# Optimization experiments

Measured on AMD Instinct MI355X. Metric: run time of the kernel, lower is better.

## Reference

```python
import jax, jax.numpy as jnp
import numpy as np

B, T, D = 2, 2048, 2048
H, KV = 16, 4
HD = D // H  # 128
ROPE_BASE = 10000.0


def _rope(t):
    # t: [B, h, T, HD]; faithful to torch apply_rope (even/odd split, concat halves)
    pos = jnp.arange(T, dtype=t.dtype)
    inv_freq = 1.0 / (ROPE_BASE ** (jnp.arange(0, HD, 2, dtype=t.dtype) / HD))
    ang = jnp.einsum('t,f->tf', pos, inv_freq)  # [T, HD/2]
    sin = jnp.sin(ang)[None, None]
    cos = jnp.cos(ang)[None, None]
    t1, t2 = t[..., ::2], t[..., 1::2]
    return jnp.concatenate([t1 * cos - t2 * sin, t1 * sin + t2 * cos], axis=-1)


def setup_inputs() -> dict:
    key = jax.random.key(0)
    kx, kq, kk, kv, ko = jax.random.split(key, 5)
    x = jax.random.normal(kx, (B, T, D), dtype=jnp.float32)
    s = 0.02
    Wq = jax.random.normal(kq, (D, D), dtype=jnp.float32) * s
    Wk = jax.random.normal(kk, (D, KV * HD), dtype=jnp.float32) * s
    Wv = jax.random.normal(kv, (D, KV * HD), dtype=jnp.float32) * s
    Wo = jax.random.normal(ko, (D, D), dtype=jnp.float32) * s
    return {"x": x, "Wq": Wq, "Wk": Wk, "Wv": Wv, "Wo": Wo}


def reference(x, Wq, Wk, Wv, Wo):
    # projections (nn.Linear, no bias)
    q = (x @ Wq).reshape(B, T, H, HD).transpose(0, 2, 1, 3)    # [B,H,T,HD]
    k = (x @ Wk).reshape(B, T, KV, HD).transpose(0, 2, 1, 3)   # [B,KV,T,HD]
    v = (x @ Wv).reshape(B, T, KV, HD).transpose(0, 2, 1, 3)
    q = _rope(q)
    k = _rope(k)
    # GQA: repeat_interleave kv heads to full head count
    g = H // KV
    k = jnp.repeat(k, g, axis=1)
    v = jnp.repeat(v, g, axis=1)
    # causal SDPA, default scale 1/sqrt(head_dim)
    scale = 1.0 / jnp.sqrt(jnp.array(HD, dtype=x.dtype))
    scores = jnp.einsum('bhqd,bhkd->bhqk', q, k) * scale
    mask = jnp.tril(jnp.ones((T, T), dtype=bool))
    scores = jnp.where(mask, scores, jnp.finfo(scores.dtype).min)
    attn = jax.nn.softmax(scores, axis=-1)
    out = jnp.einsum('bhqk,bhkd->bhqd', attn, v)               # [B,H,T,HD]
    out = out.transpose(0, 2, 1, 3).reshape(B, T, D)
    return out @ Wo
```

## Files before the change

kernel.cpp:

```cpp
#include <hip/hip_runtime.h>
#include <math.h>

#define BB 2
#define TT 2048
#define DD 2048
#define HH 16
#define KVHN 4
#define HDIM 128
#define NKV 3072

typedef unsigned short u16;
typedef unsigned int u32;
typedef __bf16 bf16x8 __attribute__((ext_vector_type(8)));
typedef float  f32x4  __attribute__((ext_vector_type(4)));

#define AS1 __attribute__((address_space(1)))
#define AS3 __attribute__((address_space(3)))

__device__ __forceinline__ void dma16(const u16* g, u16* l) {
  __builtin_amdgcn_global_load_lds((const AS1 u32*)g, (AS3 u32*)l, 16, 0, 0);
}

__device__ __forceinline__ u16 f2bf(float f) {
  u32 u = __float_as_uint(f);
  u32 r = (u + 0x7FFFu + ((u >> 16) & 1u)) >> 16;
  return (u16)r;
}
__device__ __forceinline__ float bf2f(u32 h) { return __uint_as_float(h << 16); }

__device__ __forceinline__ u32 pack2(float a, float b) {
  union { __bf16 h[2]; u32 u; } cv;
  cv.h[0] = (__bf16)a; cv.h[1] = (__bf16)b;
  return cv.u;
}

__global__ __launch_bounds__(256) void castf2b(const float* __restrict__ in,
                                               u16* __restrict__ out) {
  size_t i4 = (size_t)blockIdx.x * 256 + threadIdx.x;
  float4 v = *(const float4*)(in + i4 * 4);
  ushort4 o;
  o.x = f2bf(v.x); o.y = f2bf(v.y); o.z = f2bf(v.z); o.w = f2bf(v.w);
  *(ushort4*)(out + i4 * 4) = o;
}

__global__ __launch_bounds__(256) void tcast(const float* __restrict__ W,
                                             u16* __restrict__ WT,
                                             int K, int N) {
  __shared__ float tile[32][33];
  const int n0 = blockIdx.x * 32, k0 = blockIdx.y * 32;
  const int r = threadIdx.x >> 3;
  const int c4 = (threadIdx.x & 7) * 4;
  float4 v = *(const float4*)(W + (size_t)(k0 + r) * N + n0 + c4);
  tile[r][c4 + 0] = v.x; tile[r][c4 + 1] = v.y;
  tile[r][c4 + 2] = v.z; tile[r][c4 + 3] = v.w;
  __syncthreads();
  ushort4 o;
  o.x = f2bf(tile[c4 + 0][r]); o.y = f2bf(tile[c4 + 1][r]);
  o.z = f2bf(tile[c4 + 2][r]); o.w = f2bf(tile[c4 + 3][r]);
  *(ushort4*)(WT + (size_t)(n0 + r) * K + k0 + c4) = o;
}

template <int OUT_BF16>
__global__ __launch_bounds__(512) void gemm8p(const u16* __restrict__ A,
                                              const u16* __restrict__ BT,
                                              void* __restrict__ Cv,
                                              int N, int K) {
  __shared__ u16 lds[3 * 12288];
  const int t = threadIdx.x;
  const int l = t & 63, w = t >> 6;
  const int lm = l & 15, quad = l >> 4;
  const int wm = w & 1, wn = w >> 1;
  const int m0 = blockIdx.y * 128, n0 = blockIdx.x * 256;
  const int wu = __builtin_amdgcn_readfirstlane(w);

  const u16* srcA; int dstA;
  const u16* srcB[2]; int dstB[2];
  {
    int p0 = wu * 64, p = p0 + l;
    int row = p >> 2, c = (p & 3) ^ (row & 3);
    srcA = A + (size_t)(m0 + row) * K + c * 8;
    dstA = p0 * 8;
  }
  #pragma unroll
  for (int i = 0; i < 2; ++i) {
    int p0 = (wu * 2 + i) * 64, p = p0 + l;
    int row = p >> 2, c = (p & 3) ^ (row & 3);
    srcB[i] = BT + (size_t)(n0 + row) * K + c * 8;
    dstB[i] = 4096 + p0 * 8;
  }

  f32x4 acc[4][4];
  #pragma unroll
  for (int i = 0; i < 4; ++i)
    #pragma unroll
    for (int j = 0; j < 4; ++j) acc[i][j] = (f32x4){0.f, 0.f, 0.f, 0.f};

  auto stage = [&](int bsel) {
    u16* buf = &lds[bsel * 12288];
    dma16(srcA, buf + dstA); srcA += 32;
    #pragma unroll
    for (int i = 0; i < 2; ++i) { dma16(srcB[i], buf + dstB[i]); srcB[i] += 32; }
  };

  stage(0); stage(1); stage(2);

  const int NT = K >> 5;
  int bsel = 0;
  const int xc = lm & 3;
  for (int tI = 0; tI < NT; ++tI) {
    if (tI + 2 < NT)      asm volatile("s_waitcnt vmcnt(6)" ::: "memory");
    else if (tI + 1 < NT) asm volatile("s_waitcnt vmcnt(3)" ::: "memory");
    else                  asm volatile("s_waitcnt vmcnt(0)" ::: "memory");
    asm volatile("s_barrier" ::: "memory");

    const u16* Ab = &lds[bsel * 12288];
    const u16* Bb = Ab + 4096;
    const int ch = (quad ^ xc) * 8;
    bf16x8 a[4], b[4];
    #pragma unroll
    for (int i = 0; i < 4; ++i)
      a[i] = *(const bf16x8*)&Ab[(wm * 64 + i * 16 + lm) * 32 + ch];
    #pragma unroll
    for (int j = 0; j < 4; ++j)
      b[j] = *(const bf16x8*)&Bb[(wn * 64 + j * 16 + lm) * 32 + ch];
    __builtin_amdgcn_s_setprio(1);
    #pragma unroll
    for (int i = 0; i < 4; ++i)
      #pragma unroll
      for (int j = 0; j < 4; ++j)
        acc[i][j] = __builtin_amdgcn_mfma_f32_16x16x32_bf16(a[i], b[j], acc[i][j], 0, 0, 0);
    __builtin_amdgcn_s_setprio(0);
    asm volatile("s_barrier" ::: "memory");
    if (tI + 3 < NT) stage(bsel);
    bsel = (bsel == 2) ? 0 : bsel + 1;
  }

  #pragma unroll
  for (int i = 0; i < 4; ++i) {
    #pragma unroll
    for (int r = 0; r < 4; ++r) {
      size_t gr = (size_t)(m0 + wm * 64 + i * 16 + quad * 4 + r);
      #pragma unroll
      for (int j = 0; j < 4; ++j) {
        int gc = n0 + wn * 64 + j * 16 + lm;
        if (OUT_BF16) ((u16*)Cv)[gr * N + gc] = f2bf(acc[i][j][r]);
        else          ((float*)Cv)[gr * N + gc] = acc[i][j][r];
      }
    }
  }
}

__global__ __launch_bounds__(256) void rope2(u16* p) {
  const int row = blockIdx.x;
  const int pos = row & (TT - 1);
  u16* base = p + (size_t)row * NKV;
  float e0[5], e1[5];
  #pragma unroll
  for (int i = 0; i < 5; ++i) {
    int item = threadIdx.x + i * 256;
    int h20 = item >> 6, f = item & 63;
    int col = (h20 < 16) ? h20 * 128 : 2048 + (h20 - 16) * 128;
    u32 u = *(const u32*)(base + col + 2 * f);
    e0[i] = bf2f(u & 0xffffu);
    e1[i] = bf2f(u >> 16);
  }
  __syncthreads();
  #pragma unroll
  for (int i = 0; i < 5; ++i) {
    int item = threadIdx.x + i * 256;
    int h20 = item >> 6, f = item & 63;
    int col = (h20 < 16) ? h20 * 128 : 2048 + (h20 - 16) * 128;
    float sc = (h20 < 16) ? 0.08838834764831845f : 1.0f;
    float inv = exp2f((float)f * -0.20762050593046898f);
    float ang = (float)pos * inv;
    float sn, cs;
    sincosf(ang, &sn, &cs);
    base[col + f]      = f2bf((e0[i] * cs - e1[i] * sn) * sc);
    base[col + 64 + f] = f2bf((e0[i] * sn + e1[i] * cs) * sc);
  }
}

__global__ __launch_bounds__(256) void vtrans(const u16* __restrict__ QKV,
                                              u16* __restrict__ Vt) {
  __shared__ u16 tl[64][72];
  const int t0 = blockIdx.x * 64;
  const int y  = blockIdx.y;
  const int b  = blockIdx.z;
  #pragma unroll
  for (int i = 0; i < 2; ++i) {
    int idx = threadIdx.x + i * 256;
    int r = idx >> 3, c = (idx & 7) * 8;
    *(uint4*)&tl[r][c] =
        *(const uint4*)(QKV + (size_t)(b * TT + t0 + r) * NKV + 2560 + y * 64 + c);
  }
  __syncthreads();
  const int vh = y >> 1;
  #pragma unroll
  for (int i = 0; i < 2; ++i) {
    int idx = threadIdx.x + i * 256;
    int dr = idx >> 3, tc = (idx & 7) * 8;
    u16 tmp[8];
    #pragma unroll
    for (int j = 0; j < 8; ++j) tmp[j] = tl[tc + j][dr];
    int dloc = (y & 1) * 64 + dr;
    *(uint4*)(Vt + (size_t)((b * KVHN + vh) * HDIM + dloc) * TT + t0 + tc) =
        *(const uint4*)tmp;
  }
}

__global__ __launch_bounds__(256, 3) void attn5(const u16* __restrict__ QKV,
                                                const u16* __restrict__ Vt,
                                                u16* __restrict__ Ob) {
  __shared__ u16 Ks[3 * 4096];
  __shared__ u16 Vs[3 * 4096];
  __shared__ u16 Pw[4 * 512];
  const int t = threadIdx.x;
  const int l = t & 63, w = t >> 6;
  const int lm = l & 15, quad = l >> 4;
  const int h = blockIdx.y, b = blockIdx.z;
  const int qbase = (blockIdx.x + (blockIdx.y & 7)) & 31;
  const int qt = (blockIdx.y & 8) ? (31 - qbase) : qbase;
  const int kvh = h >> 2;
  const int q0 = qt * 64;
  const int last = 2 * qt + 1;
  const int wu = __builtin_amdgcn_readfirstlane(w);
  u16* pwv = &Pw[w * 512];
  constexpr float L2E = 1.4426950408889634f;

  bf16x8 qf[4];
  {
    size_t r0 = (size_t)(b * TT + q0 + w * 16 + lm) * NKV + h * HDIM;
    #pragma unroll
    for (int ks = 0; ks < 4; ++ks)
      qf[ks] = *(const bf16x8*)(QKV + r0 + ks * 32 + quad * 8);
  }

  f32x4 o[8];
  #pragma unroll
  for (int i = 0; i < 8; ++i) o[i] = (f32x4){0.f, 0.f, 0.f, 0.f};
  float m_ = -1e30f, l_ = 0.f;

  const u16 *kg[2], *vg[2];
  int koff[2], voff[2];
  #pragma unroll
  for (int i = 0; i < 2; ++i) {
    int p0 = (wu * 2 + i) * 64, p = p0 + l;
    int krow = p >> 4, kcp = p & 15, kcl = kcp ^ (krow & 15);
    kg[i] = QKV + (size_t)(b * TT + krow) * NKV + 2048 + kvh * HDIM + kcl * 8;
    koff[i] = p0 * 8;
    int vrow = p >> 3, vphys = p & 7, vcl = vphys ^ (vrow & 7);
    int vd = vrow + (vcl >> 2) * 64, vtch = vcl & 3;
    vg[i] = Vt + (size_t)((b * KVHN + kvh) * HDIM + vd) * TT + vtch * 8;
    voff[i] = p0 * 8;
  }

  auto stageKV = [&](int bsel) {
    u16* kd = Ks + bsel * 4096;
    u16* vd = Vs + bsel * 4096;
    #pragma unroll
    for (int i = 0; i < 2; ++i) {
      dma16(kg[i], kd + koff[i]);  kg[i] += 32 * NKV;
      dma16(vg[i], vd + voff[i]);  vg[i] += 32;
    }
  };

  stageKV(0);
  if (1 <= last) stageKV(1);
  if (2 <= last) stageKV(2);

  const int qrow = q0 + w * 16 + lm;

  int bs = 0;
  for (int kt = 0; kt <= last; ++kt) {
    if (kt + 2 <= last)      asm volatile("s_waitcnt vmcnt(8)" ::: "memory");
    else if (kt + 1 <= last) asm volatile("s_waitcnt vmcnt(4)" ::: "memory");
    else                     asm volatile("s_waitcnt vmcnt(0)" ::: "memory");
    asm volatile("s_barrier" ::: "memory");

    const u16* kcur = Ks + bs * 4096;
    const u16* vcur = Vs + bs * 4096;

    f32x4 s[2];
    s[0] = (f32x4){0.f, 0.f, 0.f, 0.f};
    s[1] = (f32x4){0.f, 0.f, 0.f, 0.f};
    __builtin_amdgcn_s_setprio(1);
    #pragma unroll
    for (int ks = 0; ks < 4; ++ks) {
      #pragma unroll
      for (int mt = 0; mt < 2; ++mt) {
        bf16x8 kb = *(const bf16x8*)&kcur[(mt * 16 + lm) * 128 + (((ks * 4 + quad) ^ lm) * 8)];
        s[mt] = __builtin_amdgcn_mfma_f32_16x16x32_bf16(kb, qf[ks], s[mt], 0, 0, 0);
      }
    }
    __builtin_amdgcn_s_setprio(0);

    if (kt >= 2 * qt) {
      #pragma unroll
      for (int mt = 0; mt < 2; ++mt)
        #pragma unroll
        for (int r = 0; r < 4; ++r) {
          int kv = kt * 32 + mt * 16 + quad * 4 + r;
          if (kv > qrow) s[mt][r] = -1e30f;
        }
    }

    float mx = -1e30f;
    #pragma unroll
    for (int mt = 0; mt < 2; ++mt)
      #pragma unroll
      for (int r = 0; r < 4; ++r) mx = fmaxf(mx, s[mt][r]);
    mx = fmaxf(mx, __shfl_xor(mx, 16));
    mx = fmaxf(mx, __shfl_xor(mx, 32));
    bool upd = mx > m_ + 8.f;
    float mn = upd ? mx : m_;
    float al = upd ? exp2f((m_ - mn) * L2E) : 1.f;
    m_ = mn;
    float sum = 0.f;
    #pragma unroll
    for (int mt = 0; mt < 2; ++mt)
      #pragma unroll
      for (int r = 0; r < 4; ++r) {
        float pv = exp2f((s[mt][r] - mn) * L2E);
        s[mt][r] = pv;
        sum += pv;
      }
    sum += __shfl_xor(sum, 16);
    sum += __shfl_xor(sum, 32);
    l_ = l_ * al + sum;

    #pragma unroll
    for (int mt = 0; mt < 2; ++mt) {
      u32 p01 = pack2(s[mt][0], s[mt][1]);
      u32 p23 = pack2(s[mt][2], s[mt][3]);
      int c = mt * 2 + (quad >> 1);
      int addr = (lm >> 1) * 64 + ((lm & 1) * 4 + (c ^ ((lm >> 1) & 3))) * 8 + (quad & 1) * 4;
      uint2 uv; uv.x = p01; uv.y = p23;
      *(uint2*)&pwv[addr] = uv;
    }
    if (__any(upd)) {
      #pragma unroll
      for (int i = 0; i < 8; ++i)
        #pragma unroll
        for (int r = 0; r < 4; ++r) o[i][r] *= al;
    }

    int paddr = (lm >> 1) * 64 + ((lm & 1) * 4 + (quad ^ ((lm >> 1) & 3))) * 8;
    bf16x8 pb = *(const bf16x8*)&pwv[paddr];
    __builtin_amdgcn_s_setprio(1);
    #pragma unroll
    for (int mt2 = 0; mt2 < 8; ++mt2) {
      int vrow = (mt2 & 3) * 16 + lm;
      int vphys = ((mt2 >> 2) * 4 + quad) ^ (vrow & 7);
      bf16x8 vb = *(const bf16x8*)&vcur[vrow * 64 + vphys * 8];
      o[mt2] = __builtin_amdgcn_mfma_f32_16x16x32_bf16(vb, pb, o[mt2], 0, 0, 0);
    }
    __builtin_amdgcn_s_setprio(0);

    asm volatile("s_barrier" ::: "memory");
    if (kt + 3 <= last) stageKV(bs);
    bs = (bs == 2) ? 0 : bs + 1;
  }

  __syncthreads();
  u16* esc = Ks + (w >> 1) * 4096 + (w & 1) * 2048;
  float inv = 1.f / l_;
  #pragma unroll
  for (int mt2 = 0; mt2 < 8; ++mt2) {
    u32 a0 = pack2(o[mt2][0] * inv, o[mt2][1] * inv);
    u32 a1 = pack2(o[mt2][2] * inv, o[mt2][3] * inv);
    int phys = (mt2 * 2 + (quad >> 1)) ^ (lm & 7);
    int addr = lm * 128 + phys * 8 + (quad & 1) * 4;
    uint2 uv; uv.x = a0; uv.y = a1;
    *(uint2*)&esc[addr] = uv;
  }
  #pragma unroll
  for (int i = 0; i < 4; ++i) {
    int p = i * 64 + l;
    int row = p >> 4, cl = p & 15;
    int cph = cl ^ (row & 7);
    uint4 val = *(const uint4*)&esc[row * 128 + cph * 8];
    *(uint4*)(Ob + (size_t)(b * TT + q0 + w * 16 + row) * DD + h * HDIM + cl * 8) = val;
  }
}

extern "C" void kernel_launch(void* const* d_in, const int* in_sizes, int n_in,
                              void* d_out, int out_size, void* d_ws, size_t ws_size,
                              hipStream_t stream) {
  const float* x  = (const float*)d_in[0];
  const float* Wq = (const float*)d_in[1];
  const float* Wk = (const float*)d_in[2];
  const float* Wv = (const float*)d_in[3];
  const float* Wo = (const float*)d_in[4];
  float* out = (float*)d_out;

  u16* xb    = (u16*)d_ws;
  u16* WqkvT = xb + 8388608;
  u16* WoT   = xb + 14680064;
  u16* Vt    = WqkvT;
  u16* Ob    = xb;
  u16* QKVb  = (u16*)d_out;

  dim3 blk(256);
  castf2b<<<8192, blk, 0, stream>>>(x, xb);
  tcast<<<dim3(64, 64), blk, 0, stream>>>(Wq, WqkvT, DD, DD);
  tcast<<<dim3(16, 64), blk, 0, stream>>>(Wk, WqkvT + (size_t)2048 * DD, DD, 512);
  tcast<<<dim3(16, 64), blk, 0, stream>>>(Wv, WqkvT + (size_t)2560 * DD, DD, 512);
  tcast<<<dim3(64, 64), blk, 0, stream>>>(Wo, WoT, DD, DD);

  gemm8p<1><<<dim3(NKV / 256, 32), dim3(512), 0, stream>>>(xb, WqkvT, QKVb, NKV, DD);
  rope2<<<BB * TT, blk, 0, stream>>>(QKVb);
  vtrans<<<dim3(32, 8, BB), blk, 0, stream>>>(QKVb, Vt);
  attn5<<<dim3(32, HH, BB), blk, 0, stream>>>(QKVb, Vt, Ob);
  gemm8p<0><<<dim3(DD / 256, 32), dim3(512), 0, stream>>>(Ob, WoT, out, DD, DD);
}
```

Baseline: 341.3 us.

## Fuse Q RoPE into attention and switch to double-buffered KV staging

The separate RoPE pass now rotates only the K heads, and Q RoPE plus the softmax scale are applied in registers when the attention kernel loads Q. The attention kernel's 3-stage LDS ring with explicit vmcnt waits becomes a 2-buffer ping-pong. The V prefetch is issued before the QK MFMAs and the K prefetch after them, and launch bounds rise to 4 blocks per CU. This removes Q read/write traffic from the RoPE kernel and cuts LDS use to allow more occupancy. In exchange the prefetch depth is shallower, and every attention block now recomputes sincos for its Q rows.

```diff
diff --git a/kernel.cpp b/kernel.cpp
--- a/kernel.cpp
+++ b/kernel.cpp
@@ -150,34 +150,22 @@
   }
 }
 
-__global__ __launch_bounds__(256) void rope2(u16* p) {
+__global__ __launch_bounds__(256) void rope2k(u16* p) {
   const int row = blockIdx.x;
   const int pos = row & (TT - 1);
-  u16* base = p + (size_t)row * NKV;
-  float e0[5], e1[5];
-  #pragma unroll
-  for (int i = 0; i < 5; ++i) {
-    int item = threadIdx.x + i * 256;
-    int h20 = item >> 6, f = item & 63;
-    int col = (h20 < 16) ? h20 * 128 : 2048 + (h20 - 16) * 128;
-    u32 u = *(const u32*)(base + col + 2 * f);
-    e0[i] = bf2f(u & 0xffffu);
-    e1[i] = bf2f(u >> 16);
-  }
+  u16* base = p + (size_t)row * NKV + 2048;
+  const int kh = threadIdx.x >> 6, f = threadIdx.x & 63;
+  const int col = kh * 128;
+  u32 u = *(const u32*)(base + col + 2 * f);
+  float e0 = bf2f(u & 0xffffu);
+  float e1 = bf2f(u >> 16);
   __syncthreads();
-  #pragma unroll
-  for (int i = 0; i < 5; ++i) {
-    int item = threadIdx.x + i * 256;
-    int h20 = item >> 6, f = item & 63;
-    int col = (h20 < 16) ? h20 * 128 : 2048 + (h20 - 16) * 128;
-    float sc = (h20 < 16) ? 0.08838834764831845f : 1.0f;
-    float inv = exp2f((float)f * -0.20762050593046898f);
-    float ang = (float)pos * inv;
-    float sn, cs;
-    sincosf(ang, &sn, &cs);
-    base[col + f]      = f2bf((e0[i] * cs - e1[i] * sn) * sc);
-    base[col + 64 + f] = f2bf((e0[i] * sn + e1[i] * cs) * sc);
-  }
+  float inv = exp2f((float)f * -0.20762050593046898f);
+  float ang = (float)pos * inv;
+  float sn, cs;
+  sincosf(ang, &sn, &cs);
+  base[col + f]      = f2bf(e0 * cs - e1 * sn);
+  base[col + 64 + f] = f2bf(e0 * sn + e1 * cs);
 }
 
 __global__ __launch_bounds__(256) void vtrans(const u16* __restrict__ QKV,
@@ -208,11 +196,11 @@
   }
 }
 
-__global__ __launch_bounds__(256, 3) void attn5(const u16* __restrict__ QKV,
+__global__ __launch_bounds__(256, 4) void attn4(const u16* __restrict__ QKV,
                                                 const u16* __restrict__ Vt,
                                                 u16* __restrict__ Ob) {
-  __shared__ u16 Ks[3 * 4096];
-  __shared__ u16 Vs[3 * 4096];
+  __shared__ u16 KsA[32 * 128], KsB[32 * 128];
+  __shared__ u16 VsA[64 * 64], VsB[64 * 64];
   __shared__ u16 Pw[4 * 512];
   const int t = threadIdx.x;
   const int l = t & 63, w = t >> 6;
@@ -227,14 +215,6 @@
   u16* pwv = &Pw[w * 512];
   constexpr float L2E = 1.4426950408889634f;
 
-  bf16x8 qf[4];
-  {
-    size_t r0 = (size_t)(b * TT + q0 + w * 16 + lm) * NKV + h * HDIM;
-    #pragma unroll
-    for (int ks = 0; ks < 4; ++ks)
-      qf[ks] = *(const bf16x8*)(QKV + r0 + ks * 32 + quad * 8);
-  }
-
   f32x4 o[8];
   #pragma unroll
   for (int i = 0; i < 8; ++i) o[i] = (f32x4){0.f, 0.f, 0.f, 0.f};
@@ -254,31 +234,45 @@
     voff[i] = p0 * 8;
   }
 
-  auto stageKV = [&](int bsel) {
-    u16* kd = Ks + bsel * 4096;
-    u16* vd = Vs + bsel * 4096;
-    #pragma unroll
-    for (int i = 0; i < 2; ++i) {
-      dma16(kg[i], kd + koff[i]);  kg[i] += 32 * NKV;
-      dma16(vg[i], vd + voff[i]);  vg[i] += 32;
-    }
-  };
-
-  stageKV(0);
-  if (1 <= last) stageKV(1);
-  if (2 <= last) stageKV(2);
+  #pragma unroll
+  for (int i = 0; i < 2; ++i) {
+    dma16(kg[i], KsA + koff[i]);
+    dma16(vg[i], VsA + voff[i]);
+    kg[i] += 32 * NKV;
+    vg[i] += 32;
+  }
 
   const int qrow = q0 + w * 16 + lm;
 
-  int bs = 0;
-  for (int kt = 0; kt <= last; ++kt) {
-    if (kt + 2 <= last)      asm volatile("s_waitcnt vmcnt(8)" ::: "memory");
-    else if (kt + 1 <= last) asm volatile("s_waitcnt vmcnt(4)" ::: "memory");
-    else                     asm volatile("s_waitcnt vmcnt(0)" ::: "memory");
-    asm volatile("s_barrier" ::: "memory");
-
-    const u16* kcur = Ks + bs * 4096;
-    const u16* vcur = Vs + bs * 4096;
+  bf16x8 qf[4];
+  {
+    const u16* qp = QKV + (size_t)(b * TT + qrow) * NKV + h * HDIM;
+    bf16x8 raw[4];
+    #pragma unroll
+    for (int i = 0; i < 4; ++i)
+      raw[i] = *(const bf16x8*)(qp + (i >> 1) * 64 + quad * 16 + (i & 1) * 8);
+    #pragma unroll
+    for (int kp = 0; kp < 2; ++kp)
+      #pragma unroll
+      for (int e = 0; e < 8; ++e) {
+        int f = kp * 32 + quad * 8 + e;
+        float ang = (float)qrow * exp2f((float)f * -0.20762050593046898f);
+        float sn, cs;
+        sincosf(ang, &sn, &cs);
+        float e0 = (float)raw[kp * 2 + (e >> 2)][(2 * e) & 7];
+        float e1 = (float)raw[kp * 2 + (e >> 2)][(2 * e + 1) & 7];
+        qf[kp][e]     = (__bf16)((e0 * cs - e1 * sn) * 0.08838834764831845f);
+        qf[kp + 2][e] = (__bf16)((e0 * sn + e1 * cs) * 0.08838834764831845f);
+      }
+  }
+
+  auto body = [&](int kt, const u16* kcur, const u16* vcur, u16* knx, u16* vnx) {
+    __syncthreads();
+    const bool pf = kt < last;
+    if (pf) {
+      #pragma unroll
+      for (int i = 0; i < 2; ++i) dma16(vg[i], vnx + voff[i]);
+    }
 
     f32x4 s[2];
     s[0] = (f32x4){0.f, 0.f, 0.f, 0.f};
@@ -293,6 +287,14 @@
       }
     }
     __builtin_amdgcn_s_setprio(0);
+    if (pf) {
+      #pragma unroll
+      for (int i = 0; i < 2; ++i) {
+        dma16(kg[i], knx + koff[i]);
+        kg[i] += 32 * NKV;
+        vg[i] += 32;
+      }
+    }
 
     if (kt >= 2 * qt) {
       #pragma unroll
@@ -355,14 +357,15 @@
       o[mt2] = __builtin_amdgcn_mfma_f32_16x16x32_bf16(vb, pb, o[mt2], 0, 0, 0);
     }
     __builtin_amdgcn_s_setprio(0);
-
-    asm volatile("s_barrier" ::: "memory");
-    if (kt + 3 <= last) stageKV(bs);
-    bs = (bs == 2) ? 0 : bs + 1;
+  };
+
+  for (int kt = 0; kt <= last; ++kt) {
+    if ((kt & 1) == 0) body(kt, KsA, VsA, KsB, VsB);
+    else               body(kt, KsB, VsB, KsA, VsA);
   }
 
   __syncthreads();
-  u16* esc = Ks + (w >> 1) * 4096 + (w & 1) * 2048;
+  u16* esc = ((w & 2) ? KsB : KsA) + (w & 1) * 2048;
   float inv = 1.f / l_;
   #pragma unroll
   for (int mt2 = 0; mt2 < 8; ++mt2) {
@@ -408,8 +411,8 @@
   tcast<<<dim3(64, 64), blk, 0, stream>>>(Wo, WoT, DD, DD);
 
   gemm8p<1><<<dim3(NKV / 256, 32), dim3(512), 0, stream>>>(xb, WqkvT, QKVb, NKV, DD);
-  rope2<<<BB * TT, blk, 0, stream>>>(QKVb);
+  rope2k<<<BB * TT, blk, 0, stream>>>(QKVb);
   vtrans<<<dim3(32, 8, BB), blk, 0, stream>>>(QKVb, Vt);
-  attn5<<<dim3(32, HH, BB), blk, 0, stream>>>(QKVb, Vt, Ob);
+  attn4<<<dim3(32, HH, BB), blk, 0, stream>>>(QKVb, Vt, Ob);
   gemm8p<0><<<dim3(DD / 256, 32), dim3(512), 0, stream>>>(Ob, WoT, out, DD, DD);
 }
```

Result: faster. 325.1 us (-4.8%).
